# Optimization experiments

Hardware: AMD Instinct MI355X
Metric: run time of the kernel (lower is better)

## Reference

```python
import jax, jax.numpy as jnp
import numpy as np


def _margins(labels):
    # labels: [B, L] int. Imposter index j = roll(i+1, wrap).
    lab_j = jnp.roll(labels, -1, axis=0)
    equal = jnp.all(labels == lab_j, axis=1)                 # [B]
    n = jnp.sum(labels | lab_j, axis=1).astype(jnp.float32)  # union count
    diff = jnp.sum(labels ^ lab_j, axis=1).astype(jnp.float32)
    margin = jnp.maximum(0.5, diff / jnp.maximum(n, 1.0))
    return jnp.where(equal, 0.0, margin)                     # [B]


def setup_inputs() -> dict:
    key = jax.random.key(0)
    k1, k2, k3 = jax.random.split(key, 3)
    B, D, L = 16384, 512, 14
    z_image = jax.random.normal(k1, (B, D), dtype=jnp.float32)
    z_text = jax.random.normal(k2, (B, D), dtype=jnp.float32)
    labels = jax.random.randint(k3, (B, L), 0, 2, dtype=jnp.int32)
    return {"z_image": z_image, "z_text": z_text, "labels": labels}


def reference(z_image, z_text, labels):
    # similarity_function='dot' (default in forward call sites)
    B = z_image.shape[0]
    margin = _margins(labels)                                 # [B]
    paired = jnp.sum(z_image * z_text, axis=1)                # [B] dot(z_image[i], z_text[i])
    zi_j = jnp.roll(z_image, -1, axis=0)                      # z_image[j]
    zt_j = jnp.roll(z_text, -1, axis=0)                       # z_text[j]
    imp_img = jnp.sum(zi_j * z_text, axis=1)                  # dot(z_image[j], z_text[i])
    imp_txt = jnp.sum(zt_j * z_image, axis=1)                 # dot(z_text[j], z_image[i])
    loss_img = jnp.sum(jnp.maximum(imp_img - paired + margin, 0.0)) / B
    loss_txt = jnp.sum(jnp.maximum(imp_txt - paired + margin, 0.0)) / B
    return (loss_img + loss_txt).reshape(1)
```

## Files before the change

kernel.cpp:

```cpp
#include <hip/hip_runtime.h>


constexpr int B = 16384;
constexpr int L = 14;
constexpr int BLOCK = 256;
constexpr int R = 8;
constexpr int STRIPS_PER_BLOCK = 2;
constexpr int GRID = B / (STRIPS_PER_BLOCK * R);

__device__ __forceinline__ float dot4(float4 a, float4 b) {
    return a.x * b.x + a.y * b.y + a.z * b.z + a.w * b.w;
}

__global__ __launch_bounds__(BLOCK) void rank_main(
    const float* __restrict__ zi, const float* __restrict__ zt,
    const int* __restrict__ labels, float* __restrict__ ws)
{
    const int lane = threadIdx.x & 63;
    const int wv   = threadIdx.x >> 6;
    const int pair = wv >> 1;
    const int half = wv & 1;
    const int base = (blockIdx.x * STRIPS_PER_BLOCK + pair) * R;

    const float4* zi4 = (const float4*)zi;
    const float4* zt4 = (const float4*)zt;

    __shared__ float sdot[4][R][3];
    __shared__ float smar[STRIPS_PER_BLOCK][R];

    size_t o = (size_t)base * 128 + half * 64 + lane;
    float4 a = zi4[o];
    float4 b = zt4[o];
    int lab = (half == 0 && lane < L) ? labels[base * L + lane] : 0;
    float pd = dot4(a, b);

    #pragma unroll
    for (int r = 0; r < R; ++r) {
        const int nrow = (base + r + 1) & (B - 1);
        const size_t no = (size_t)nrow * 128 + half * 64 + lane;
        const float4 na = zi4[no];
        const float4 nb = zt4[no];
        const int nlab = (half == 0 && lane < L) ? labels[nrow * L + lane] : 0;

        float s0 = pd;
        float s1 = dot4(na, b);
        float s2 = dot4(nb, a);
        const float npd = dot4(na, nb);

        if (half == 0) {
            const unsigned long long bor  = __ballot((lab | nlab) != 0);
            const unsigned long long bxor = __ballot((lab ^ nlab) != 0);
            if (lane == 0) {
                const int df = __popcll(bxor);
                float margin = 0.0f;
                if (df != 0)
                    margin = fmaxf(0.5f, (float)df / (float)__popcll(bor));
                smar[pair][r] = margin;
            }
        }

        #pragma unroll
        for (int off = 32; off > 0; off >>= 1) {
            s0 += __shfl_down(s0, off);
            s1 += __shfl_down(s1, off);
            s2 += __shfl_down(s2, off);
        }
        if (lane == 0) {
            sdot[wv][r][0] = s0;
            sdot[wv][r][1] = s1;
            sdot[wv][r][2] = s2;
        }

        a = na; b = nb; lab = nlab; pd = npd;
    }

    __syncthreads();

    const int t = threadIdx.x;
    float hinge = 0.0f;
    if (t < STRIPS_PER_BLOCK * R) {
        const int p = t >> 3, r = t & 7;
        const float q0 = sdot[p * 2][r][0] + sdot[p * 2 + 1][r][0];
        const float q1 = sdot[p * 2][r][1] + sdot[p * 2 + 1][r][1];
        const float q2 = sdot[p * 2][r][2] + sdot[p * 2 + 1][r][2];
        const float m  = smar[p][r];
        hinge = fmaxf(q1 - q0 + m, 0.0f) + fmaxf(q2 - q0 + m, 0.0f);
    }
    #pragma unroll
    for (int off = 8; off > 0; off >>= 1) hinge += __shfl_down(hinge, off);
    if (t == 0) ws[blockIdx.x] = hinge;
}

__global__ __launch_bounds__(BLOCK) void rank_reduce(
    const float* __restrict__ ws, float* __restrict__ out)
{
    const int t = threadIdx.x;
    float v = ws[t] + ws[t + 256] + ws[t + 512] + ws[t + 768];
    #pragma unroll
    for (int off = 32; off > 0; off >>= 1) v += __shfl_down(v, off);
    __shared__ float s[4];
    if ((t & 63) == 0) s[t >> 6] = v;
    __syncthreads();
    if (t == 0)
        out[0] = (s[0] + s[1] + s[2] + s[3]) * (1.0f / (float)B);
}

extern "C" void kernel_launch(void* const* d_in, const int* in_sizes, int n_in,
                              void* d_out, int out_size, void* d_ws, size_t ws_size,
                              hipStream_t stream) {
    const float* zi     = (const float*)d_in[0];
    const float* zt     = (const float*)d_in[1];
    const int*   labels = (const int*)d_in[2];
    float* out = (float*)d_out;
    float* ws  = (float*)d_ws;

    rank_main<<<GRID, BLOCK, 0, stream>>>(zi, zt, labels, ws);
    rank_reduce<<<1, BLOCK, 0, stream>>>(ws, out);
}
```

Measured before the change: 99.57 us.

## Halve rows per strip, remap blocks across XCDs, prefetch two rows ahead

Cuts rows per strip from 8 to 4, which doubles the grid to 2048 blocks. It also remaps block indices so consecutive row ranges land on the same XCD, aiming for better L2 locality when neighbouring strips reread boundary rows. The row loop now software-prefetches the row two ahead, giving more loads in flight. The trade-offs are more boundary rows read twice and more partials for the reduce kernel to sum.

```diff
diff --git a/kernel.cpp b/kernel.cpp
--- a/kernel.cpp
+++ b/kernel.cpp
@@ -4,9 +4,11 @@
 constexpr int B = 16384;
 constexpr int L = 14;
 constexpr int BLOCK = 256;
-constexpr int R = 8;
-constexpr int STRIPS_PER_BLOCK = 2;
-constexpr int GRID = B / (STRIPS_PER_BLOCK * R);
+constexpr int R = 4;
+constexpr int SPB = 2;
+constexpr int GRID = B / (SPB * R);
+constexpr int NXCD = 8;
+constexpr int CPX = GRID / NXCD;
 
 __device__ __forceinline__ float dot4(float4 a, float4 b) {
     return a.x * b.x + a.y * b.y + a.z * b.z + a.w * b.w;
@@ -20,27 +22,37 @@
     const int wv   = threadIdx.x >> 6;
     const int pair = wv >> 1;
     const int half = wv & 1;
-    const int base = (blockIdx.x * STRIPS_PER_BLOCK + pair) * R;
+    const int bid  = (int)(blockIdx.x & (NXCD - 1)) * CPX + (int)(blockIdx.x >> 3);
+    const int base = (bid * SPB + pair) * R;
 
     const float4* zi4 = (const float4*)zi;
     const float4* zt4 = (const float4*)zt;
 
     __shared__ float sdot[4][R][3];
-    __shared__ float smar[STRIPS_PER_BLOCK][R];
+    __shared__ float smar[SPB][R];
 
-    size_t o = (size_t)base * 128 + half * 64 + lane;
-    float4 a = zi4[o];
-    float4 b = zt4[o];
-    int lab = (half == 0 && lane < L) ? labels[base * L + lane] : 0;
+    const int col = half * 64 + lane;
+    const size_t o = (size_t)base * 128 + col;
+
+    float4 a = zi4[o], b = zt4[o];
+    const int r1 = (base + 1) & (B - 1);
+    float4 na = zi4[(size_t)r1 * 128 + col];
+    float4 nb = zt4[(size_t)r1 * 128 + col];
+    int lab  = (half == 0 && lane < L) ? labels[base * L + lane] : 0;
+    int nlab = (half == 0 && lane < L) ? labels[r1 * L + lane] : 0;
     float pd = dot4(a, b);
 
     #pragma unroll
     for (int r = 0; r < R; ++r) {
-        const int nrow = (base + r + 1) & (B - 1);
-        const size_t no = (size_t)nrow * 128 + half * 64 + lane;
-        const float4 na = zi4[no];
-        const float4 nb = zt4[no];
-        const int nlab = (half == 0 && lane < L) ? labels[nrow * L + lane] : 0;
+        float4 fa = make_float4(0.f, 0.f, 0.f, 0.f), fb = fa;
+        int flab = 0;
+        if (r < R - 1) {
+            const int frow = (base + r + 2) & (B - 1);
+            const size_t fo = (size_t)frow * 128 + col;
+            fa = zi4[fo];
+            fb = zt4[fo];
+            if (half == 0 && lane < L) flab = labels[frow * L + lane];
+        }
 
         float s0 = pd;
         float s1 = dot4(na, b);
@@ -71,15 +83,16 @@
             sdot[wv][r][2] = s2;
         }
 
-        a = na; b = nb; lab = nlab; pd = npd;
+        a = na; b = nb; na = fa; nb = fb;
+        lab = nlab; nlab = flab; pd = npd;
     }
 
     __syncthreads();
 
     const int t = threadIdx.x;
     float hinge = 0.0f;
-    if (t < STRIPS_PER_BLOCK * R) {
-        const int p = t >> 3, r = t & 7;
+    if (t < SPB * R) {
+        const int p = t >> 2, r = t & 3;
         const float q0 = sdot[p * 2][r][0] + sdot[p * 2 + 1][r][0];
         const float q1 = sdot[p * 2][r][1] + sdot[p * 2 + 1][r][1];
         const float q2 = sdot[p * 2][r][2] + sdot[p * 2 + 1][r][2];
@@ -87,7 +100,7 @@
         hinge = fmaxf(q1 - q0 + m, 0.0f) + fmaxf(q2 - q0 + m, 0.0f);
     }
     #pragma unroll
-    for (int off = 8; off > 0; off >>= 1) hinge += __shfl_down(hinge, off);
+    for (int off = 4; off > 0; off >>= 1) hinge += __shfl_down(hinge, off);
     if (t == 0) ws[blockIdx.x] = hinge;
 }
 
@@ -95,7 +108,9 @@
     const float* __restrict__ ws, float* __restrict__ out)
 {
     const int t = threadIdx.x;
-    float v = ws[t] + ws[t + 256] + ws[t + 512] + ws[t + 768];
+    float v = 0.0f;
+    #pragma unroll
+    for (int k = 0; k < GRID / BLOCK; ++k) v += ws[t + k * BLOCK];
     #pragma unroll
     for (int off = 32; off > 0; off >>= 1) v += __shfl_down(v, off);
     __shared__ float s[4];
```

New measurement: 100.0 us. About the same (+0.5%).
